# Kernel tuning notes

Measured on AMD Instinct MI355X. Metric: run time of the kernel, lower is better.

The kernel has to match this reference:

```python
import jax, jax.numpy as jnp
import numpy as np

DIM = 1024
NUM_HEADS = 16
HEAD_DIM = DIM // NUM_HEADS
SCALE = HEAD_DIM ** -0.5


def setup_inputs() -> dict:
    key = jax.random.key(0)
    ks = jax.random.split(key, 7)
    s = DIM ** -0.5
    return {
        "x": jax.random.normal(ks[0], (4, 2048, DIM), dtype=jnp.float32),
        "wq": jax.random.normal(ks[1], (DIM, DIM), dtype=jnp.float32) * s,
        "wk": jax.random.normal(ks[2], (DIM, DIM), dtype=jnp.float32) * s,
        "wv": jax.random.normal(ks[3], (DIM, DIM), dtype=jnp.float32) * s,
        "wo": jax.random.normal(ks[4], (DIM, DIM), dtype=jnp.float32) * s,
        "bo": jax.random.normal(ks[5], (DIM,), dtype=jnp.float32) * 0.02,
    }


def reference(x, wq, wk, wv, wo, bo):
    B, N, C = x.shape
    H, D = NUM_HEADS, HEAD_DIM
    # projections (qkv_bias=False); weights stored as [out, in] like nn.Linear
    q = jnp.einsum("bnc,oc->bno", x, wq).reshape(B, N, H, D).transpose(0, 2, 1, 3)
    k = jnp.einsum("bnc,oc->bno", x, wk).reshape(B, N, H, D).transpose(0, 2, 1, 3)
    v = jnp.einsum("bnc,oc->bno", x, wv).reshape(B, N, H, D).transpose(0, 2, 1, 3)
    # full NxN scores, scaled after the matmul as in the original
    scores = jnp.einsum("bhqd,bhkd->bhqk", q, k) * SCALE
    probs = jax.nn.softmax(scores, axis=-1)  # attn_drop is identity (p=0, eval)
    out = jnp.einsum("bhqk,bhkd->bhqd", probs, v)
    out = out.transpose(0, 2, 1, 3).reshape(B, N, C)
    # output projection with bias; proj_drop identity
    return jnp.einsum("bnc,oc->bno", out, wo) + bo
```

## Files before the change

### kernel.cpp

```cpp
#include <hip/hip_runtime.h>

typedef unsigned short u16;
typedef __attribute__((ext_vector_type(8))) short short8;
typedef __attribute__((ext_vector_type(4))) float f32x4;

#define LOG2E 1.44269504088896340736f

__device__ __forceinline__ u16 f2bf(float f) {
    unsigned u = __float_as_uint(f);
    u += 0x7fffu + ((u >> 16) & 1u);
    return (u16)(u >> 16);
}

__device__ __forceinline__ void async_cp16(const void* g, void* l) {
    __builtin_amdgcn_global_load_lds(
        (const __attribute__((address_space(1))) unsigned*)g,
        (__attribute__((address_space(3))) unsigned*)l, 16, 0, 0);
}

__device__ __forceinline__ unsigned pack_trunc(float a, float b) {
    return __builtin_amdgcn_perm(__float_as_uint(b), __float_as_uint(a), 0x07060302u);
}

__global__ void cast_all(const float4* __restrict__ x,
                         const float4* __restrict__ wq, const float4* __restrict__ wk,
                         const float4* __restrict__ wv, const float4* __restrict__ wo,
                         uint2* __restrict__ xb, uint2* __restrict__ wqkv,
                         uint2* __restrict__ wob) {
    long long g = (long long)blockIdx.x * blockDim.x + threadIdx.x;
    const long long XG = (8192LL * 1024) / 4;
    const long long WN = (1024LL * 1024) / 4;
    float4 v;
    uint2* dst;
    if (g < XG) {
        v = x[g];
        dst = xb + g;
    } else {
        long long t = g - XG;
        int s = (int)(t / WN);
        long long r = t - (long long)s * WN;
        const float4* src = (s == 0) ? wq : (s == 1) ? wk : (s == 2) ? wv : wo;
        v = src[r];
        dst = (s < 3) ? (wqkv + (long long)s * WN + r) : (wob + r);
    }
    uint2 p;
    p.x = (unsigned)f2bf(v.x) | ((unsigned)f2bf(v.y) << 16);
    p.y = (unsigned)f2bf(v.z) | ((unsigned)f2bf(v.w) << 16);
    *dst = p;
}

template <int MODE>
__global__ __launch_bounds__(256, 2) void gemm_nt(
    const u16* __restrict__ A, const u16* __restrict__ Bw,
    u16* __restrict__ Qo, u16* __restrict__ Ko, u16* __restrict__ Vto,
    float* __restrict__ Fo, const float* __restrict__ bias, int K) {
    __shared__ u16 As[128 * 64];
    __shared__ u16 Bs[128 * 64];

    const int tid = threadIdx.x;
    const int lane = tid & 63, wave = tid >> 6;
    const int wm = wave >> 1, wn = wave & 1;
    const int quad = lane >> 4, l16 = lane & 15;
    const long long m0 = (long long)blockIdx.y * 128;
    const long long n0 = (long long)blockIdx.x * 128;

    f32x4 acc[4][4];
#pragma unroll
    for (int i = 0; i < 4; i++)
#pragma unroll
        for (int j = 0; j < 4; j++) acc[i][j] = (f32x4){0.f, 0.f, 0.f, 0.f};

    for (int kt = 0; kt < K; kt += 64) {
#pragma unroll
        for (int i = 0; i < 4; i++) {
            int ff = i * 256 + tid;
            int row = ff >> 3, c = ff & 7;
            int gc = c ^ (row & 7);
            async_cp16(A + (m0 + row) * K + kt + gc * 8, &As[ff * 8]);
            async_cp16(Bw + (n0 + row) * K + kt + gc * 8, &Bs[ff * 8]);
        }
        __syncthreads();
#pragma unroll
        for (int ks = 0; ks < 2; ks++) {
            short8 af[4], bfr[4];
#pragma unroll
            for (int t = 0; t < 4; t++) {
                int rowA = wm * 64 + t * 16 + l16;
                int ca = (ks * 4 + quad) ^ (rowA & 7);
                af[t] = *(const short8*)(&As[rowA * 64 + ca * 8]);
                int rowB = wn * 64 + t * 16 + l16;
                int cb = (ks * 4 + quad) ^ (rowB & 7);
                bfr[t] = *(const short8*)(&Bs[rowB * 64 + cb * 8]);
            }
#pragma unroll
            for (int i = 0; i < 4; i++)
#pragma unroll
                for (int j = 0; j < 4; j++)
                    acc[i][j] = __builtin_amdgcn_mfma_f32_16x16x32_bf16(
                        af[i], bfr[j], acc[i][j], 0, 0, 0);
        }
        __syncthreads();
    }

#pragma unroll
    for (int i = 0; i < 4; i++) {
        int mg = (int)m0 + wm * 64 + i * 16 + quad * 4;
#pragma unroll
        for (int j = 0; j < 4; j++) {
            int ng = (int)n0 + wn * 64 + j * 16 + l16;
            f32x4 v = acc[i][j];
            if (MODE == 0) {
                int which = ng >> 10;
                int wi = ng & 1023;
                int h = wi >> 6, d = wi & 63;
                int b = mg >> 11;
                int seq = mg & 2047;
                long long bh = (long long)(b * 16 + h);
                if (which == 0) {
                    const float QS = 0.125f * LOG2E;
                    u16* dst = Qo + (bh * 2048 + seq) * 64 + d;
#pragma unroll
                    for (int r = 0; r < 4; r++) dst[r * 64] = f2bf(v[r] * QS);
                } else if (which == 1) {
                    u16* dst = Ko + (bh * 2048 + seq) * 64 + d;
#pragma unroll
                    for (int r = 0; r < 4; r++) dst[r * 64] = f2bf(v[r]);
                } else {
                    u16* dst = Vto + (bh * 64 + d) * 2048 + seq;
                    uint2 p;
                    p.x = (unsigned)f2bf(v[0]) | ((unsigned)f2bf(v[1]) << 16);
                    p.y = (unsigned)f2bf(v[2]) | ((unsigned)f2bf(v[3]) << 16);
                    *(uint2*)dst = p;
                }
            } else {
                float* dst = Fo + (long long)mg * 1024 + ng;
                float bb = bias[ng];
#pragma unroll
                for (int r = 0; r < 4; r++) dst[r * 1024] = v[r] + bb;
            }
        }
    }
}

__global__ __launch_bounds__(512, 4) void attn(
    const u16* __restrict__ Q, const u16* __restrict__ Kb,
    const u16* __restrict__ Vt, u16* __restrict__ O) {
    __shared__ u16 Ks[2][64 * 64];
    __shared__ u16 Vs[2][64 * 64];
    __shared__ u16 Ps[8][32 * 64];

    const int tid = threadIdx.x;
    const int lane = tid & 63, wave = tid >> 6;
    const int quad = lane >> 4, l16 = lane & 15;
    const int qt = blockIdx.x, bh = blockIdx.y;

    const u16* Qh = Q + (long long)bh * 2048 * 64;
    const u16* Kh = Kb + (long long)bh * 2048 * 64;
    const u16* Vh = Vt + (long long)bh * 64 * 2048;
    const int q0 = qt * 256 + wave * 32;

    const int srow = tid >> 3, sc = tid & 7;
    const int sgc = sc ^ (srow & 7);
    const u16* Kg = Kh + srow * 64 + sgc * 8;
    const u16* Vg = Vh + (long long)srow * 2048 + sgc * 8;

    short8 qf[2][2];
#pragma unroll
    for (int tm = 0; tm < 2; tm++)
#pragma unroll
        for (int ks = 0; ks < 2; ks++)
            qf[tm][ks] = *(const short8*)(Qh + (q0 + tm * 16 + l16) * 64 + ks * 32 + quad * 8);

    u16* Pw = &Ps[wave][0];
    int pwr[2][4], prd[2][2], kvo[2][4];
#pragma unroll
    for (int tm = 0; tm < 2; tm++) {
        const int qrow = tm * 16 + l16;
#pragma unroll
        for (int tn = 0; tn < 4; tn++)
            pwr[tm][tn] = qrow * 64 + (((tn * 2 + (quad >> 1)) ^ (l16 & 7)) * 8) + 4 * (quad & 1);
#pragma unroll
        for (int ks = 0; ks < 2; ks++)
            prd[tm][ks] = qrow * 64 + (((ks * 4 + quad) ^ (l16 & 7)) * 8);
    }
#pragma unroll
    for (int ks = 0; ks < 2; ks++)
#pragma unroll
        for (int tn = 0; tn < 4; tn++) {
            int row = tn * 16 + l16;
            kvo[ks][tn] = row * 64 + (((ks * 4 + quad) ^ (row & 7)) * 8);
        }

    f32x4 o_acc[2][4], lacc[2];
#pragma unroll
    for (int tm = 0; tm < 2; tm++) {
        lacc[tm] = (f32x4){0.f, 0.f, 0.f, 0.f};
#pragma unroll
        for (int tn = 0; tn < 4; tn++) o_acc[tm][tn] = (f32x4){0.f, 0.f, 0.f, 0.f};
    }
    const float NEGC = -12.0f * LOG2E;
    const short BF1 = (short)0x3F80;
    const short8 ones = {BF1, BF1, BF1, BF1, BF1, BF1, BF1, BF1};

    async_cp16(Kg, &Ks[0][tid * 8]);
    async_cp16(Vg, &Vs[0][tid * 8]);

#define ATTN_STEP(KT, BUF)                                                              \
    do {                                                                                \
        __syncthreads();                                                                \
        if ((KT) < 31) {                                                                \
            async_cp16(Kg + ((KT) + 1) * 4096, &Ks[(BUF) ^ 1][tid * 8]);                \
            async_cp16(Vg + ((KT) + 1) * 64, &Vs[(BUF) ^ 1][tid * 8]);                  \
        }                                                                               \
        const u16* Kc = &Ks[BUF][0];                                                    \
        const u16* Vc = &Vs[BUF][0];                                                    \
        f32x4 s[2][4];                                                                  \
        _Pragma("unroll") for (int tm = 0; tm < 2; tm++)                                \
            _Pragma("unroll") for (int tn = 0; tn < 4; tn++)                            \
                s[tm][tn] = (f32x4){NEGC, NEGC, NEGC, NEGC};                            \
        _Pragma("unroll") for (int ks = 0; ks < 2; ks++) {                              \
            short8 kf[4];                                                               \
            _Pragma("unroll") for (int tn = 0; tn < 4; tn++)                            \
                kf[tn] = *(const short8*)(&Kc[kvo[ks][tn]]);                            \
            _Pragma("unroll") for (int tm = 0; tm < 2; tm++)                            \
                _Pragma("unroll") for (int tn = 0; tn < 4; tn++)                        \
                    s[tm][tn] = __builtin_amdgcn_mfma_f32_16x16x32_bf16(                \
                        kf[tn], qf[tm][ks], s[tm][tn], 0, 0, 0);                        \
        }                                                                               \
        _Pragma("unroll") for (int tm = 0; tm < 2; tm++)                                \
            _Pragma("unroll") for (int tn = 0; tn < 4; tn++) {                          \
                f32x4 sv = s[tm][tn];                                                   \
                float p0 = __builtin_amdgcn_exp2f(sv[0]);                               \
                float p1 = __builtin_amdgcn_exp2f(sv[1]);                               \
                float p2 = __builtin_amdgcn_exp2f(sv[2]);                               \
                float p3 = __builtin_amdgcn_exp2f(sv[3]);                               \
                uint2 pk;                                                               \
                pk.x = pack_trunc(p0, p1);                                              \
                pk.y = pack_trunc(p2, p3);                                              \
                *(uint2*)(&Pw[pwr[tm][tn]]) = pk;                                       \
            }                                                                           \
        _Pragma("unroll") for (int ks = 0; ks < 2; ks++) {                              \
            short8 vf[4];                                                               \
            _Pragma("unroll") for (int tn = 0; tn < 4; tn++)                            \
                vf[tn] = *(const short8*)(&Vc[kvo[ks][tn]]);                            \
            short8 pf0 = *(const short8*)(&Pw[prd[0][ks]]);                             \
            short8 pf1 = *(const short8*)(&Pw[prd[1][ks]]);                             \
            lacc[0] = __builtin_amdgcn_mfma_f32_16x16x32_bf16(pf0, ones, lacc[0], 0, 0, 0); \
            lacc[1] = __builtin_amdgcn_mfma_f32_16x16x32_bf16(pf1, ones, lacc[1], 0, 0, 0); \
            _Pragma("unroll") for (int tn = 0; tn < 4; tn++) {                          \
                o_acc[0][tn] = __builtin_amdgcn_mfma_f32_16x16x32_bf16(                 \
                    pf0, vf[tn], o_acc[0][tn], 0, 0, 0);                                \
                o_acc[1][tn] = __builtin_amdgcn_mfma_f32_16x16x32_bf16(                 \
                    pf1, vf[tn], o_acc[1][tn], 0, 0, 0);                                \
            }                                                                           \
        }                                                                               \
    } while (0)

#pragma unroll 1
    for (int kt = 0; kt < 32; kt += 2) {
        ATTN_STEP(kt, 0);
        ATTN_STEP(kt + 1, 1);
    }
#undef ATTN_STEP

    f32x4 linv[2];
#pragma unroll
    for (int tm = 0; tm < 2; tm++)
#pragma unroll
        for (int r = 0; r < 4; r++) linv[tm][r] = 1.0f / lacc[tm][r];

    const int b = bh >> 4, h = bh & 15;
#pragma unroll
    for (int tm = 0; tm < 2; tm++)
#pragma unroll
        for (int tn = 0; tn < 4; tn++) {
            int seq = q0 + tm * 16 + quad * 4;
            int c = h * 64 + tn * 16 + l16;
            u16* dst = O + ((long long)(b * 2048 + seq)) * 1024 + c;
#pragma unroll
            for (int r = 0; r < 4; r++)
                dst[r * 1024] = f2bf(o_acc[tm][tn][r] * linv[tm][r]);
        }
}

extern "C" void kernel_launch(void* const* d_in, const int* in_sizes, int n_in,
                              void* d_out, int out_size, void* d_ws, size_t ws_size,
                              hipStream_t stream) {
    const float* x = (const float*)d_in[0];
    const float* wq = (const float*)d_in[1];
    const float* wk = (const float*)d_in[2];
    const float* wv = (const float*)d_in[3];
    const float* wo = (const float*)d_in[4];
    const float* bo = (const float*)d_in[5];
    float* out = (float*)d_out;

    char* ws = (char*)d_ws;
    u16* xb   = (u16*)(ws);
    u16* wqkv = (u16*)(ws + (16LL << 20));
    u16* wob  = (u16*)(ws + (22LL << 20));
    u16* Qb   = (u16*)(ws + (24LL << 20));
    u16* Kbuf = (u16*)(ws + (40LL << 20));
    u16* Vt   = (u16*)(ws + (56LL << 20));
    u16* Ob   = (u16*)(ws + (72LL << 20));

    cast_all<<<12288, 256, 0, stream>>>((const float4*)x, (const float4*)wq,
                                        (const float4*)wk, (const float4*)wv,
                                        (const float4*)wo, (uint2*)xb,
                                        (uint2*)wqkv, (uint2*)wob);

    dim3 g1(24, 64);
    gemm_nt<0><<<g1, 256, 0, stream>>>(xb, wqkv, Qb, Kbuf, Vt, nullptr, nullptr, 1024);

    dim3 g2(8, 64);
    attn<<<g2, 512, 0, stream>>>(Qb, Kbuf, Vt, Ob);

    dim3 g3(8, 64);
    gemm_nt<1><<<g3, 256, 0, stream>>>(Ob, wob, nullptr, nullptr, nullptr, out, bo, 1024);
}
```

Baseline: 259.5 us.

## Feed softmax probabilities to PV MFMA directly from registers, dropping LDS round-trip

The exponentiated score tiles are packed into bf16x4 register fragments and used straight away as the A operand of 16x16x16 bf16 MFMAs. Before, they were written to a per-wave shared-memory buffer and read back as 16x16x32 fragments. This removes the P LDS buffer along with its stores and loads, which frees shared memory and may raise occupancy. The cost is that the PV and row-sum products now use twice as many half-K MFMA instructions, and V is read from LDS in smaller 8-byte fragments with a new swizzled offset table.

```diff
diff --git a/kernel.cpp b/kernel.cpp
--- a/kernel.cpp
+++ b/kernel.cpp
@@ -2,6 +2,7 @@
 
 typedef unsigned short u16;
 typedef __attribute__((ext_vector_type(8))) short short8;
+typedef __attribute__((ext_vector_type(4))) short bf16x4;
 typedef __attribute__((ext_vector_type(4))) float f32x4;
 
 #define LOG2E 1.44269504088896340736f
@@ -147,7 +148,6 @@
     const u16* __restrict__ Vt, u16* __restrict__ O) {
     __shared__ u16 Ks[2][64 * 64];
     __shared__ u16 Vs[2][64 * 64];
-    __shared__ u16 Ps[8][32 * 64];
 
     const int tid = threadIdx.x;
     const int lane = tid & 63, wave = tid >> 6;
@@ -171,18 +171,7 @@
         for (int ks = 0; ks < 2; ks++)
             qf[tm][ks] = *(const short8*)(Qh + (q0 + tm * 16 + l16) * 64 + ks * 32 + quad * 8);
 
-    u16* Pw = &Ps[wave][0];
-    int pwr[2][4], prd[2][2], kvo[2][4];
-#pragma unroll
-    for (int tm = 0; tm < 2; tm++) {
-        const int qrow = tm * 16 + l16;
-#pragma unroll
-        for (int tn = 0; tn < 4; tn++)
-            pwr[tm][tn] = qrow * 64 + (((tn * 2 + (quad >> 1)) ^ (l16 & 7)) * 8) + 4 * (quad & 1);
-#pragma unroll
-        for (int ks = 0; ks < 2; ks++)
-            prd[tm][ks] = qrow * 64 + (((ks * 4 + quad) ^ (l16 & 7)) * 8);
-    }
+    int kvo[2][4];
 #pragma unroll
     for (int ks = 0; ks < 2; ks++)
 #pragma unroll
@@ -190,6 +179,14 @@
             int row = tn * 16 + l16;
             kvo[ks][tn] = row * 64 + (((ks * 4 + quad) ^ (row & 7)) * 8);
         }
+    int vro[4][4];
+#pragma unroll
+    for (int tn = 0; tn < 4; tn++)
+#pragma unroll
+        for (int dt = 0; dt < 4; dt++) {
+            int row = dt * 16 + l16;
+            vro[tn][dt] = row * 64 + (((tn * 2 + (quad >> 1)) ^ (l16 & 7)) * 8) + (quad & 1) * 4;
+        }
 
     f32x4 o_acc[2][4], lacc[2];
 #pragma unroll
@@ -200,7 +197,7 @@
     }
     const float NEGC = -12.0f * LOG2E;
     const short BF1 = (short)0x3F80;
-    const short8 ones = {BF1, BF1, BF1, BF1, BF1, BF1, BF1, BF1};
+    const bf16x4 ones4 = {BF1, BF1, BF1, BF1};
 
     async_cp16(Kg, &Ks[0][tid * 8]);
     async_cp16(Vg, &Vs[0][tid * 8]);
@@ -227,6 +224,7 @@
                     s[tm][tn] = __builtin_amdgcn_mfma_f32_16x16x32_bf16(                \
                         kf[tn], qf[tm][ks], s[tm][tn], 0, 0, 0);                        \
         }                                                                               \
+        bf16x4 paf[2][4];                                                               \
         _Pragma("unroll") for (int tm = 0; tm < 2; tm++)                                \
             _Pragma("unroll") for (int tn = 0; tn < 4; tn++) {                          \
                 f32x4 sv = s[tm][tn];                                                   \
@@ -237,22 +235,20 @@
                 uint2 pk;                                                               \
                 pk.x = pack_trunc(p0, p1);                                              \
                 pk.y = pack_trunc(p2, p3);                                              \
-                *(uint2*)(&Pw[pwr[tm][tn]]) = pk;                                       \
+                paf[tm][tn] = *(bf16x4*)&pk;                                            \
             }                                                                           \
-        _Pragma("unroll") for (int ks = 0; ks < 2; ks++) {                              \
-            short8 vf[4];                                                               \
-            _Pragma("unroll") for (int tn = 0; tn < 4; tn++)                            \
-                vf[tn] = *(const short8*)(&Vc[kvo[ks][tn]]);                            \
-            short8 pf0 = *(const short8*)(&Pw[prd[0][ks]]);                             \
-            short8 pf1 = *(const short8*)(&Pw[prd[1][ks]]);                             \
-            lacc[0] = __builtin_amdgcn_mfma_f32_16x16x32_bf16(pf0, ones, lacc[0], 0, 0, 0); \
-            lacc[1] = __builtin_amdgcn_mfma_f32_16x16x32_bf16(pf1, ones, lacc[1], 0, 0, 0); \
-            _Pragma("unroll") for (int tn = 0; tn < 4; tn++) {                          \
-                o_acc[0][tn] = __builtin_amdgcn_mfma_f32_16x16x32_bf16(                 \
-                    pf0, vf[tn], o_acc[0][tn], 0, 0, 0);                                \
-                o_acc[1][tn] = __builtin_amdgcn_mfma_f32_16x16x32_bf16(                 \
-                    pf1, vf[tn], o_acc[1][tn], 0, 0, 0);                                \
+        _Pragma("unroll") for (int tn = 0; tn < 4; tn++) {                              \
+            _Pragma("unroll") for (int dt = 0; dt < 4; dt++) {                          \
+                bf16x4 vf4 = *(const bf16x4*)(&Vc[vro[tn][dt]]);                        \
+                o_acc[0][dt] = __builtin_amdgcn_mfma_f32_16x16x16bf16_1k(               \
+                    paf[0][tn], vf4, o_acc[0][dt], 0, 0, 0);                            \
+                o_acc[1][dt] = __builtin_amdgcn_mfma_f32_16x16x16bf16_1k(               \
+                    paf[1][tn], vf4, o_acc[1][dt], 0, 0, 0);                            \
             }                                                                           \
+            lacc[0] = __builtin_amdgcn_mfma_f32_16x16x16bf16_1k(                        \
+                paf[0][tn], ones4, lacc[0], 0, 0, 0);                                   \
+            lacc[1] = __builtin_amdgcn_mfma_f32_16x16x16bf16_1k(                        \
+                paf[1][tn], ones4, lacc[1], 0, 0, 0);                                   \
         }                                                                               \
     } while (0)
 
```

Result: faster. 250.8 us (-3.4%).
